# Kernel optimization log

Measured on AMD Instinct MI355X. Metric: run time of the kernel, lower is better.

## Reference

```python
import math
import jax, jax.numpy as jnp
import numpy as np

DIM_K = 64  # init arg: softmax scaling dimension


def setup_inputs() -> dict:
    k = jax.random.key(0)
    k1, k2, k3 = jax.random.split(k, 3)
    B, H, S, D = 4, 16, 4096, 64
    return {
        "query": jax.random.normal(k1, (B, H, S, D), dtype=jnp.float32),
        "key": jax.random.normal(k2, (B, H, S, D), dtype=jnp.float32),
        "value": jax.random.normal(k3, (B, H, S, D), dtype=jnp.float32),
        "causal_mask": 1,
    }


def reference(query, key, value, causal_mask):
    B, H, Q, dk = query.shape
    S = key.shape[2]
    dv = value.shape[-1]
    q = query / math.sqrt(DIM_K)
    chunk = max(1, min(int(math.sqrt(S)), S))
    n_chunks = S // chunk  # S chosen divisible by chunk
    neg_inf = jnp.float32(-jnp.inf)

    # [n_chunks, B, H, chunk, d]
    k_chunks = jnp.moveaxis(key.reshape(B, H, n_chunks, chunk, dk), 2, 0)
    v_chunks = jnp.moveaxis(value.reshape(B, H, n_chunks, chunk, dv), 2, 0)
    qpos = jnp.arange(Q)

    def step(carry, inputs):
        value_sum, normalizer, max_score = carry
        k_ch, v_ch, c_idx = inputs
        scores = jnp.einsum("bhqd,bhkd->bhqk", q, k_ch)  # [B,H,Q,chunk]
        if causal_mask:
            kpos = c_idx * chunk + jnp.arange(chunk)
            mask = qpos[:, None] >= kpos[None, :]
            scores = jnp.where(mask[None, None], scores, neg_inf)
        max_prev = max_score
        max_score = jnp.maximum(max_score, scores.max(axis=-1))
        exp_chunk = jnp.exp(scores - max_score[..., None])
        exp_prev = jnp.exp(max_prev - max_score)
        value_sum = value_sum * exp_prev[..., None] + jnp.einsum(
            "bhqk,bhkd->bhqd", exp_chunk, v_ch
        )
        normalizer = normalizer * exp_prev + exp_chunk.sum(axis=-1)
        return (value_sum, normalizer, max_score), None

    init = (
        jnp.zeros((B, H, Q, dv), dtype=query.dtype),
        jnp.zeros((B, H, Q), dtype=query.dtype),
        jnp.full((B, H, Q), neg_inf, dtype=query.dtype),
    )
    (value_sum, normalizer, _), _ = jax.lax.scan(
        step, init, (k_chunks, v_chunks, jnp.arange(n_chunks))
    )
    return value_sum / normalizer[..., None]
```

## Files before the change

### kernel.cpp

```cpp
#include <hip/hip_runtime.h>
#include <hip/hip_bf16.h>

typedef __attribute__((ext_vector_type(8))) __bf16 bf16x8;
typedef __attribute__((ext_vector_type(4))) float floatx4;

#define S_LEN 4096
#define NBH   64
#define BM    256
#define BN    64
#define PH    128
#define KSTR  72
#define VSTR  136
#define C_SCALE 0.18033688011112042f
#define RESCALE_THR 8.0f

__device__ __forceinline__ short f2bf(float x) {
  __hip_bfloat16 h = __float2bfloat16(x);
  return *reinterpret_cast<const short*>(&h);
}

__global__ __launch_bounds__(512)
void mea_fwd(const float* __restrict__ qp, const float* __restrict__ kp,
             const float* __restrict__ vp, const int* __restrict__ cm,
             float* __restrict__ op)
{
  __shared__ short kL[2][PH * KSTR];
  __shared__ short vT[2][64 * VSTR];

  const int t    = threadIdx.x;
  const int w    = t >> 6;
  const int lane = t & 63;
  const int lg   = lane >> 4;
  const int l16  = lane & 15;

  const int bh  = blockIdx.y;
  const int qt  = (int)(gridDim.x - 1) - (int)blockIdx.x;
  const int q0  = qt * BM;
  const int qw0 = q0 + w * 32;
  const long base = (long)bh * S_LEN * 64;
  const int causal = cm[0];

  const int skr = t >> 3;
  const int sd0 = (t & 7) * 8;
  const int pcol = ((skr >> 4) & 1) * 32 + ((skr >> 3) & 1) * 16 +
                   ((skr >> 2) & 1) * 8  + ((skr >> 5) & 1) * 4 + (skr & 3);
  const int svcol = (pcol + (sd0 >> 4) * 16) & 63;

  bf16x8 qfrag[2][2];
#pragma unroll
  for (int nt = 0; nt < 2; ++nt)
#pragma unroll
    for (int ks = 0; ks < 2; ++ks) {
      const float* qr = qp + base + (long)(qw0 + nt*16 + l16) * 64 + ks*32 + lg*8;
      float4 a = *(const float4*)(qr);
      float4 b = *(const float4*)(qr + 4);
      union { short s[8]; bf16x8 v; } u;
      u.s[0]=f2bf(a.x*C_SCALE); u.s[1]=f2bf(a.y*C_SCALE);
      u.s[2]=f2bf(a.z*C_SCALE); u.s[3]=f2bf(a.w*C_SCALE);
      u.s[4]=f2bf(b.x*C_SCALE); u.s[5]=f2bf(b.y*C_SCALE);
      u.s[6]=f2bf(b.z*C_SCALE); u.s[7]=f2bf(b.w*C_SCALE);
      qfrag[nt][ks] = u.v;
    }

  floatx4 oacc[2][4];
#pragma unroll
  for (int i = 0; i < 2; ++i)
#pragma unroll
    for (int j = 0; j < 4; ++j)
      oacc[i][j] = (floatx4){0.f, 0.f, 0.f, 0.f};

  float m_run[2] = {-__builtin_inff(), -__builtin_inff()};
  float l_run[2] = {0.f, 0.f};

  const int kmax = causal ? (q0 + BM) : S_LEN;
  const int nph  = kmax / PH;

  float4 kpre[2][2], vpre[2][2];
  {
    const float* kb = kp + base + (long)skr * 64 + sd0;
    kpre[0][0] = ((const float4*)kb)[0];          kpre[0][1] = ((const float4*)kb)[1];
    kpre[1][0] = ((const float4*)(kb + 4096))[0]; kpre[1][1] = ((const float4*)(kb + 4096))[1];
    const float* vb = vp + base + (long)skr * 64 + sd0;
    vpre[0][0] = ((const float4*)vb)[0];          vpre[0][1] = ((const float4*)vb)[1];
    vpre[1][0] = ((const float4*)(vb + 4096))[0]; vpre[1][1] = ((const float4*)(vb + 4096))[1];
  }

  int cur = 0;
  for (int ph = 0; ph < nph; ++ph) {

#pragma unroll
    for (int h = 0; h < 2; ++h) {
      union { short s[8]; uint4 u; } pk;
      pk.s[0]=f2bf(kpre[h][0].x); pk.s[1]=f2bf(kpre[h][0].y);
      pk.s[2]=f2bf(kpre[h][0].z); pk.s[3]=f2bf(kpre[h][0].w);
      pk.s[4]=f2bf(kpre[h][1].x); pk.s[5]=f2bf(kpre[h][1].y);
      pk.s[6]=f2bf(kpre[h][1].z); pk.s[7]=f2bf(kpre[h][1].w);
      *(uint4*)(&kL[cur][(h*64 + skr) * KSTR + sd0]) = pk.u;

      short vs[8];
      vs[0]=f2bf(vpre[h][0].x); vs[1]=f2bf(vpre[h][0].y);
      vs[2]=f2bf(vpre[h][0].z); vs[3]=f2bf(vpre[h][0].w);
      vs[4]=f2bf(vpre[h][1].x); vs[5]=f2bf(vpre[h][1].y);
      vs[6]=f2bf(vpre[h][1].z); vs[7]=f2bf(vpre[h][1].w);
#pragma unroll
      for (int i = 0; i < 8; ++i)
        vT[cur][(sd0 + i) * VSTR + h*64 + svcol] = vs[i];
    }
    __syncthreads();

    if (ph + 1 < nph) {
      const int kn = (ph + 1) * PH;
      const float* kb = kp + base + (long)(kn + skr) * 64 + sd0;
      kpre[0][0] = ((const float4*)kb)[0];          kpre[0][1] = ((const float4*)kb)[1];
      kpre[1][0] = ((const float4*)(kb + 4096))[0]; kpre[1][1] = ((const float4*)(kb + 4096))[1];
      const float* vb = vp + base + (long)(kn + skr) * 64 + sd0;
      vpre[0][0] = ((const float4*)vb)[0];          vpre[0][1] = ((const float4*)vb)[1];
      vpre[1][0] = ((const float4*)(vb + 4096))[0]; vpre[1][1] = ((const float4*)(vb + 4096))[1];
    }

    const short* kb_ = kL[cur];
    const short* vb_ = vT[cur];

#pragma unroll
    for (int sub = 0; sub < 2; ++sub) {
      const int k0 = ph * PH + sub * 64;
      if (causal && k0 >= qw0 + 32) continue;

      floatx4 sacc[4][2];
#pragma unroll
      for (int mt = 0; mt < 4; ++mt)
#pragma unroll
        for (int nt = 0; nt < 2; ++nt)
          sacc[mt][nt] = (floatx4){0.f, 0.f, 0.f, 0.f};
#pragma unroll
      for (int ks = 0; ks < 2; ++ks)
#pragma unroll
        for (int mt = 0; mt < 4; ++mt) {
          bf16x8 kfrag = *(const bf16x8*)(&kb_[(sub*64 + mt*16 + l16) * KSTR + ks*32 + lg*8]);
#pragma unroll
          for (int nt = 0; nt < 2; ++nt)
            sacc[mt][nt] = __builtin_amdgcn_mfma_f32_16x16x32_bf16(kfrag, qfrag[nt][ks], sacc[mt][nt], 0, 0, 0);
        }

      const bool needmask = causal && (k0 + BN - 1 > qw0);
      float pmax[2] = {-__builtin_inff(), -__builtin_inff()};
#pragma unroll
      for (int mt = 0; mt < 4; ++mt)
#pragma unroll
        for (int nt = 0; nt < 2; ++nt)
#pragma unroll
          for (int r = 0; r < 4; ++r) {
            float v = sacc[mt][nt][r];
            if (needmask) {
              int key = k0  + mt*16 + lg*4 + r;
              int q   = qw0 + nt*16 + l16;
              if (q < key) v = -__builtin_inff();
            }
            sacc[mt][nt][r] = v;
            pmax[nt] = fmaxf(pmax[nt], v);
          }

      const bool nore = __all(fmaxf(pmax[0] - m_run[0], pmax[1] - m_run[1]) <= RESCALE_THR);
      if (!nore) {
#pragma unroll
        for (int nt = 0; nt < 2; ++nt) {
          pmax[nt] = fmaxf(pmax[nt], __shfl_xor(pmax[nt], 16));
          pmax[nt] = fmaxf(pmax[nt], __shfl_xor(pmax[nt], 32));
        }
        float alpha[2];
#pragma unroll
        for (int nt = 0; nt < 2; ++nt) {
          float mnew = fmaxf(m_run[nt], pmax[nt]);
          alpha[nt]  = __builtin_amdgcn_exp2f(m_run[nt] - mnew);
          m_run[nt]  = mnew;
          l_run[nt] *= alpha[nt];
        }
#pragma unroll
        for (int mo = 0; mo < 2; ++mo)
#pragma unroll
          for (int r = 0; r < 4; ++r) {
            float al = __shfl(alpha[mo], lg*4 + r);
#pragma unroll
            for (int nd = 0; nd < 4; ++nd)
              oacc[mo][nd][r] *= al;
          }
      }

      bf16x8 pfrag[2][2];
      float rsum[2] = {0.f, 0.f};
#pragma unroll
      for (int nt = 0; nt < 2; ++nt)
#pragma unroll
        for (int ks = 0; ks < 2; ++ks) {
          union { short s[8]; bf16x8 v; } pk;
#pragma unroll
          for (int r = 0; r < 4; ++r) {
            float e0 = __builtin_amdgcn_exp2f(sacc[ks][nt][r]     - m_run[nt]);
            float e1 = __builtin_amdgcn_exp2f(sacc[ks + 2][nt][r] - m_run[nt]);
            rsum[nt] += e0 + e1;
            pk.s[r]     = f2bf(e0);
            pk.s[4 + r] = f2bf(e1);
          }
          pfrag[nt][ks] = pk.v;
        }
#pragma unroll
      for (int nt = 0; nt < 2; ++nt)
        l_run[nt] += rsum[nt];

#pragma unroll
      for (int ks = 0; ks < 2; ++ks) {
        bf16x8 vfrag[4];
#pragma unroll
        for (int nd = 0; nd < 4; ++nd) {
          int colr = (ks*32 + lg*8 + nd*16) & 63;
          vfrag[nd] = *(const bf16x8*)(&vb_[(nd*16 + l16) * VSTR + sub*64 + colr]);
        }
#pragma unroll
        for (int mo = 0; mo < 2; ++mo)
#pragma unroll
          for (int nd = 0; nd < 4; ++nd)
            oacc[mo][nd] = __builtin_amdgcn_mfma_f32_16x16x32_bf16(pfrag[mo][ks], vfrag[nd], oacc[mo][nd], 0, 0, 0);
      }
    }

    cur ^= 1;
  }

#pragma unroll
  for (int nt = 0; nt < 2; ++nt) {
    l_run[nt] += __shfl_xor(l_run[nt], 16);
    l_run[nt] += __shfl_xor(l_run[nt], 32);
  }
#pragma unroll
  for (int mo = 0; mo < 2; ++mo)
#pragma unroll
    for (int r = 0; r < 4; ++r) {
      float lv  = __shfl(l_run[mo], lg*4 + r);
      float inv = __builtin_amdgcn_rcpf(lv);
      int qrow  = qw0 + mo*16 + lg*4 + r;
#pragma unroll
      for (int nd = 0; nd < 4; ++nd)
        op[base + (long)qrow * 64 + nd*16 + l16] = oacc[mo][nd][r] * inv;
    }
}

extern "C" void kernel_launch(void* const* d_in, const int* in_sizes, int n_in,
                              void* d_out, int out_size, void* d_ws, size_t ws_size,
                              hipStream_t stream) {
  const float* q = (const float*)d_in[0];
  const float* k = (const float*)d_in[1];
  const float* v = (const float*)d_in[2];
  const int*  cm = (const int*)d_in[3];
  float* o = (float*)d_out;
  dim3 grid(S_LEN / BM, NBH);
  mea_fwd<<<grid, dim3(512, 1, 1), 0, stream>>>(q, k, v, cm, o);
}
```

Measured before the change: 574.9 us.

## Shrink KV phase to 64 keys and defer PV MFMA by one tile

The KV staging phase drops from 128 to 64 keys, with the shared-memory K and V buffers shrunk to match. The P·V MFMA for each tile is now deferred to the next iteration and issued after that tile's Q·K MFMAs, so the matrix work can overlap the softmax exp and conversion code; a final drain applies the last pending tile. The aim is to hide softmax latency behind matrix instructions. In exchange it adds a second __syncthreads per iteration and halves the keys processed per barrier, and the deferred P fragments raise register pressure.

New measurement: 612.3 us. +6.5%, slower.

```diff
diff --git a/kernel.cpp b/kernel.cpp
--- a/kernel.cpp
+++ b/kernel.cpp
@@ -8,9 +8,8 @@
 #define NBH   64
 #define BM    256
 #define BN    64
-#define PH    128
 #define KSTR  72
-#define VSTR  136
+#define VSTR  72
 #define C_SCALE 0.18033688011112042f
 #define RESCALE_THR 8.0f
 
@@ -24,7 +23,7 @@
              const float* __restrict__ vp, const int* __restrict__ cm,
              float* __restrict__ op)
 {
-  __shared__ short kL[2][PH * KSTR];
+  __shared__ short kL[2][BN * KSTR];
   __shared__ short vT[2][64 * VSTR];
 
   const int t    = threadIdx.x;
@@ -73,60 +72,55 @@
   float l_run[2] = {0.f, 0.f};
 
   const int kmax = causal ? (q0 + BM) : S_LEN;
-  const int nph  = kmax / PH;
-
-  float4 kpre[2][2], vpre[2][2];
+  const int nph  = kmax / BN;
+
+  float4 kpre[2], vpre[2];
   {
     const float* kb = kp + base + (long)skr * 64 + sd0;
-    kpre[0][0] = ((const float4*)kb)[0];          kpre[0][1] = ((const float4*)kb)[1];
-    kpre[1][0] = ((const float4*)(kb + 4096))[0]; kpre[1][1] = ((const float4*)(kb + 4096))[1];
+    kpre[0] = ((const float4*)kb)[0];  kpre[1] = ((const float4*)kb)[1];
     const float* vb = vp + base + (long)skr * 64 + sd0;
-    vpre[0][0] = ((const float4*)vb)[0];          vpre[0][1] = ((const float4*)vb)[1];
-    vpre[1][0] = ((const float4*)(vb + 4096))[0]; vpre[1][1] = ((const float4*)(vb + 4096))[1];
-  }
-
+    vpre[0] = ((const float4*)vb)[0];  vpre[1] = ((const float4*)vb)[1];
+  }
+
+  bf16x8 pfrag_prev[2][2];
+  bool have_prev = false;
+  int prevbuf = 0;
   int cur = 0;
-  for (int ph = 0; ph < nph; ++ph) {
-
-#pragma unroll
-    for (int h = 0; h < 2; ++h) {
+
+  for (int p = 0; p < nph; ++p) {
+
+    {
       union { short s[8]; uint4 u; } pk;
-      pk.s[0]=f2bf(kpre[h][0].x); pk.s[1]=f2bf(kpre[h][0].y);
-      pk.s[2]=f2bf(kpre[h][0].z); pk.s[3]=f2bf(kpre[h][0].w);
-      pk.s[4]=f2bf(kpre[h][1].x); pk.s[5]=f2bf(kpre[h][1].y);
-      pk.s[6]=f2bf(kpre[h][1].z); pk.s[7]=f2bf(kpre[h][1].w);
-      *(uint4*)(&kL[cur][(h*64 + skr) * KSTR + sd0]) = pk.u;
+      pk.s[0]=f2bf(kpre[0].x); pk.s[1]=f2bf(kpre[0].y);
+      pk.s[2]=f2bf(kpre[0].z); pk.s[3]=f2bf(kpre[0].w);
+      pk.s[4]=f2bf(kpre[1].x); pk.s[5]=f2bf(kpre[1].y);
+      pk.s[6]=f2bf(kpre[1].z); pk.s[7]=f2bf(kpre[1].w);
+      *(uint4*)(&kL[cur][skr * KSTR + sd0]) = pk.u;
 
       short vs[8];
-      vs[0]=f2bf(vpre[h][0].x); vs[1]=f2bf(vpre[h][0].y);
-      vs[2]=f2bf(vpre[h][0].z); vs[3]=f2bf(vpre[h][0].w);
-      vs[4]=f2bf(vpre[h][1].x); vs[5]=f2bf(vpre[h][1].y);
-      vs[6]=f2bf(vpre[h][1].z); vs[7]=f2bf(vpre[h][1].w);
+      vs[0]=f2bf(vpre[0].x); vs[1]=f2bf(vpre[0].y);
+      vs[2]=f2bf(vpre[0].z); vs[3]=f2bf(vpre[0].w);
+      vs[4]=f2bf(vpre[1].x); vs[5]=f2bf(vpre[1].y);
+      vs[6]=f2bf(vpre[1].z); vs[7]=f2bf(vpre[1].w);
 #pragma unroll
       for (int i = 0; i < 8; ++i)
-        vT[cur][(sd0 + i) * VSTR + h*64 + svcol] = vs[i];
+        vT[cur][(sd0 + i) * VSTR + svcol] = vs[i];
     }
     __syncthreads();
 
-    if (ph + 1 < nph) {
-      const int kn = (ph + 1) * PH;
+    if (p + 1 < nph) {
+      const int kn = (p + 1) * BN;
       const float* kb = kp + base + (long)(kn + skr) * 64 + sd0;
-      kpre[0][0] = ((const float4*)kb)[0];          kpre[0][1] = ((const float4*)kb)[1];
-      kpre[1][0] = ((const float4*)(kb + 4096))[0]; kpre[1][1] = ((const float4*)(kb + 4096))[1];
+      kpre[0] = ((const float4*)kb)[0];  kpre[1] = ((const float4*)kb)[1];
       const float* vb = vp + base + (long)(kn + skr) * 64 + sd0;
-      vpre[0][0] = ((const float4*)vb)[0];          vpre[0][1] = ((const float4*)vb)[1];
-      vpre[1][0] = ((const float4*)(vb + 4096))[0]; vpre[1][1] = ((const float4*)(vb + 4096))[1];
-    }
-
-    const short* kb_ = kL[cur];
-    const short* vb_ = vT[cur];
-
-#pragma unroll
-    for (int sub = 0; sub < 2; ++sub) {
-      const int k0 = ph * PH + sub * 64;
-      if (causal && k0 >= qw0 + 32) continue;
-
-      floatx4 sacc[4][2];
+      vpre[0] = ((const float4*)vb)[0];  vpre[1] = ((const float4*)vb)[1];
+    }
+
+    const int  k0  = p * BN;
+    const bool act = !(causal && k0 >= qw0 + 32);
+
+    floatx4 sacc[4][2];
+    if (act) {
 #pragma unroll
       for (int mt = 0; mt < 4; ++mt)
 #pragma unroll
@@ -136,12 +130,32 @@
       for (int ks = 0; ks < 2; ++ks)
 #pragma unroll
         for (int mt = 0; mt < 4; ++mt) {
-          bf16x8 kfrag = *(const bf16x8*)(&kb_[(sub*64 + mt*16 + l16) * KSTR + ks*32 + lg*8]);
+          bf16x8 kfrag = *(const bf16x8*)(&kL[cur][(mt*16 + l16) * KSTR + ks*32 + lg*8]);
 #pragma unroll
           for (int nt = 0; nt < 2; ++nt)
             sacc[mt][nt] = __builtin_amdgcn_mfma_f32_16x16x32_bf16(kfrag, qfrag[nt][ks], sacc[mt][nt], 0, 0, 0);
         }
-
+    }
+
+    if (have_prev) {
+#pragma unroll
+      for (int ks = 0; ks < 2; ++ks) {
+        bf16x8 vfrag[4];
+#pragma unroll
+        for (int nd = 0; nd < 4; ++nd) {
+          int colr = (ks*32 + lg*8 + nd*16) & 63;
+          vfrag[nd] = *(const bf16x8*)(&vT[cur ^ 1][(nd*16 + l16) * VSTR + colr]);
+        }
+#pragma unroll
+        for (int mo = 0; mo < 2; ++mo)
+#pragma unroll
+          for (int nd = 0; nd < 4; ++nd)
+            oacc[mo][nd] = __builtin_amdgcn_mfma_f32_16x16x32_bf16(pfrag_prev[mo][ks], vfrag[nd], oacc[mo][nd], 0, 0, 0);
+      }
+      have_prev = false;
+    }
+
+    if (act) {
       const bool needmask = causal && (k0 + BN - 1 > qw0);
       float pmax[2] = {-__builtin_inff(), -__builtin_inff()};
 #pragma unroll
@@ -186,7 +200,6 @@
           }
       }
 
-      bf16x8 pfrag[2][2];
       float rsum[2] = {0.f, 0.f};
 #pragma unroll
       for (int nt = 0; nt < 2; ++nt)
@@ -201,29 +214,35 @@
             pk.s[r]     = f2bf(e0);
             pk.s[4 + r] = f2bf(e1);
           }
-          pfrag[nt][ks] = pk.v;
+          pfrag_prev[nt][ks] = pk.v;
         }
 #pragma unroll
       for (int nt = 0; nt < 2; ++nt)
         l_run[nt] += rsum[nt];
 
-#pragma unroll
-      for (int ks = 0; ks < 2; ++ks) {
-        bf16x8 vfrag[4];
-#pragma unroll
-        for (int nd = 0; nd < 4; ++nd) {
-          int colr = (ks*32 + lg*8 + nd*16) & 63;
-          vfrag[nd] = *(const bf16x8*)(&vb_[(nd*16 + l16) * VSTR + sub*64 + colr]);
-        }
-#pragma unroll
-        for (int mo = 0; mo < 2; ++mo)
-#pragma unroll
-          for (int nd = 0; nd < 4; ++nd)
-            oacc[mo][nd] = __builtin_amdgcn_mfma_f32_16x16x32_bf16(pfrag[mo][ks], vfrag[nd], oacc[mo][nd], 0, 0, 0);
+      have_prev = true;
+      prevbuf   = cur;
+    }
+
+    __syncthreads();
+    cur ^= 1;
+  }
+
+  if (have_prev) {
+#pragma unroll
+    for (int ks = 0; ks < 2; ++ks) {
+      bf16x8 vfrag[4];
+#pragma unroll
+      for (int nd = 0; nd < 4; ++nd) {
+        int colr = (ks*32 + lg*8 + nd*16) & 63;
+        vfrag[nd] = *(const bf16x8*)(&vT[prevbuf][(nd*16 + l16) * VSTR + colr]);
       }
-    }
-
-    cur ^= 1;
+#pragma unroll
+      for (int mo = 0; mo < 2; ++mo)
+#pragma unroll
+        for (int nd = 0; nd < 4; ++nd)
+          oacc[mo][nd] = __builtin_amdgcn_mfma_f32_16x16x32_bf16(pfrag_prev[mo][ks], vfrag[nd], oacc[mo][nd], 0, 0, 0);
+    }
   }
 
 #pragma unroll
```
